# Optimization experiments

Hardware: AMD Instinct MI355X
Metric: run time of the kernel (lower is better)

The kernel has to match this reference:

```python
import jax, jax.numpy as jnp
import numpy as np

HIDDEN = 2048
NUM_HEADS = 32
NUM_KV_HEADS = 4
HEAD_DIM = 128
EPS = 1e-6
ROPE_THETA = 10000.0
Q_SIZE = NUM_HEADS * HEAD_DIM      # 4096
KV_SIZE = NUM_KV_HEADS * HEAD_DIM  # 512


def setup_inputs() -> dict:
    key = jax.random.key(0)
    k1, k2, k3, k4, k5 = jax.random.split(key, 5)
    T = 2048
    hidden_states = jax.random.normal(k1, (T, HIDDEN), dtype=jnp.float32)
    positions = jnp.arange(T, dtype=jnp.int64)
    # qkv_proj weight: [q_size + 2*kv_size, hidden] (torch Linear convention)
    w_qkv = jax.random.normal(k2, (Q_SIZE + 2 * KV_SIZE, HIDDEN), dtype=jnp.float32) * (HIDDEN ** -0.5)
    # o_proj weight: [hidden, num_heads*head_dim]
    w_o = jax.random.normal(k3, (HIDDEN, Q_SIZE), dtype=jnp.float32) * (Q_SIZE ** -0.5)
    q_norm_w = jnp.ones((HEAD_DIM,), dtype=jnp.float32) + 0.1 * jax.random.normal(k4, (HEAD_DIM,), dtype=jnp.float32)
    k_norm_w = jnp.ones((HEAD_DIM,), dtype=jnp.float32) + 0.1 * jax.random.normal(k5, (HEAD_DIM,), dtype=jnp.float32)
    return {"positions": positions, "hidden_states": hidden_states,
            "w_qkv": w_qkv, "w_o": w_o, "q_norm_w": q_norm_w, "k_norm_w": k_norm_w}


def _rms_norm(x, w):
    # x: [..., head_dim]; normalize over last dim
    var = jnp.mean(jnp.square(x), axis=-1, keepdims=True)
    return x * jax.lax.rsqrt(var + EPS) * w


def _rope(positions, x):
    # neox-style rotary over full head_dim. x: [T, H, D]
    half = HEAD_DIM // 2
    inv_freq = 1.0 / (ROPE_THETA ** (jnp.arange(0, half, dtype=jnp.float32) / half))
    freqs = positions.astype(jnp.float32)[:, None] * inv_freq[None, :]  # [T, half]
    cos = jnp.cos(freqs)[:, None, :]  # [T, 1, half]
    sin = jnp.sin(freqs)[:, None, :]
    x1, x2 = x[..., :half], x[..., half:]
    return jnp.concatenate([x1 * cos - x2 * sin, x2 * cos + x1 * sin], axis=-1)


def reference(positions, hidden_states, w_qkv, w_o, q_norm_w, k_norm_w):
    T = hidden_states.shape[0]
    qkv = hidden_states @ w_qkv.T  # [T, q_size+2*kv_size]
    q, k, v = jnp.split(qkv, [Q_SIZE, Q_SIZE + KV_SIZE], axis=-1)
    q = _rms_norm(q.reshape(T, NUM_HEADS, HEAD_DIM), q_norm_w)
    k = _rms_norm(k.reshape(T, NUM_KV_HEADS, HEAD_DIM), k_norm_w)
    v = v.reshape(T, NUM_KV_HEADS, HEAD_DIM)
    q = _rope(positions, q)
    k = _rope(positions, k)
    # GQA: expand kv heads to query heads
    rep = NUM_HEADS // NUM_KV_HEADS
    k = jnp.repeat(k, rep, axis=1)  # [T, H, D]
    v = jnp.repeat(v, rep, axis=1)
    scale = HEAD_DIM ** -0.5
    scores = jnp.einsum('qhd,khd->hqk', q, k) * scale  # [H, T, T]
    causal = jnp.tril(jnp.ones((T, T), dtype=bool))
    scores = jnp.where(causal[None, :, :], scores, jnp.float32(-1e30))
    probs = jax.nn.softmax(scores, axis=-1)
    attn = jnp.einsum('hqk,khd->qhd', probs, v).reshape(T, Q_SIZE)
    return attn @ w_o.T  # [T, hidden]
```

## Files before the change

### kernel.cpp

```cpp
#include <hip/hip_runtime.h>

#define T_TOK   2048
#define HID     2048
#define NHEADS  32
#define NKV     4
#define HD      128
#define QSZ     4096
#define KVSZ    512
#define QKVW    5120

typedef unsigned short u16;
typedef __bf16 bf16x8 __attribute__((ext_vector_type(8)));
typedef float  f32x4  __attribute__((ext_vector_type(4)));

__device__ __forceinline__ u16 f2bf(float f) {
  unsigned int u = __float_as_uint(f);
  u += 0x7fffu + ((u >> 16) & 1u);
  return (u16)(u >> 16);
}

__device__ __forceinline__ u16 f2bf_n(float f) {
  __bf16 h = (__bf16)f;
  return __builtin_bit_cast(u16, h);
}

__device__ __forceinline__ float bf2f(u16 u) {
  return __uint_as_float((unsigned int)u << 16);
}

__device__ __forceinline__ void gl2lds16(const void* g, void* l) {
  __builtin_amdgcn_global_load_lds(
      (const __attribute__((address_space(1))) unsigned int*)g,
      (__attribute__((address_space(3))) unsigned int*)l, 16, 0, 0);
}

template<int N>
__device__ __forceinline__ float rotmax(float x) {
  int t = __builtin_amdgcn_mov_dpp(__float_as_int(x), 0x120 | N, 0xf, 0xf, true);
  return fmaxf(x, __int_as_float(t));
}
template<int N>
__device__ __forceinline__ float rotadd(float x) {
  int t = __builtin_amdgcn_mov_dpp(__float_as_int(x), 0x120 | N, 0xf, 0xf, true);
  return x + __int_as_float(t);
}

__global__ void cvt3_f32_bf16(const float* __restrict__ in0, u16* __restrict__ o0, int n0,
                              const float* __restrict__ in1, u16* __restrict__ o1, int n1,
                              const float* __restrict__ in2, u16* __restrict__ o2, int n2) {
  int i = blockIdx.x * blockDim.x + threadIdx.x;
  const float* in; u16* out;
  if (i < n0)            { in = in0; out = o0; }
  else if (i < n0 + n1)  { in = in1; out = o1; i -= n0; }
  else if (i < n0+n1+n2) { in = in2; out = o2; i -= n0 + n1; }
  else return;
  float4 v = ((const float4*)in)[i];
  ushort4 o;
  o.x = f2bf(v.x); o.y = f2bf(v.y); o.z = f2bf(v.z); o.w = f2bf(v.w);
  ((ushort4*)out)[i] = o;
}

template<int BM, bool OUT16>
__launch_bounds__(256, 4)
__global__ void gemm_nt(const u16* __restrict__ A, const u16* __restrict__ B,
                        void* __restrict__ Cv, int M, int N, int K) {
  constexpr int MI = BM / 32;
  __shared__ __align__(16) u16 As[2][BM * 32];
  __shared__ __align__(16) u16 Bs[2][128 * 32];
  const int tid  = threadIdx.x;
  const int wave = tid >> 6, lane = tid & 63;
  const int l15  = lane & 15, quad = lane >> 4;
  const int wr   = wave >> 1, wc = wave & 1;

  const int nwg = gridDim.x * gridDim.y;
  int lid = blockIdx.y * gridDim.x + blockIdx.x;
  lid = (lid & 7) * (nwg >> 3) + (lid >> 3);
  const int bx = lid % gridDim.x;
  const int by = lid / gridDim.x;

  const u16* Ab = A + (size_t)by * BM * K;
  const u16* Bb = B + (size_t)bx * 128 * K;

  f32x4 acc[MI][4];
#pragma unroll
  for (int i = 0; i < MI; i++)
#pragma unroll
    for (int j = 0; j < 4; j++) acc[i][j] = (f32x4){0.f, 0.f, 0.f, 0.f};

  constexpr int ACH = BM * 32 / 8;
  auto stage = [&](int t, int buf) {
    const int k0 = t * 32;
#pragma unroll
    for (int s = 0; s < (ACH + 512) / 256; s++) {
      int c = tid + s * 256;
      if (c < ACH) {
        int row = c >> 2, co = (c & 3) * 8;
        gl2lds16(Ab + (size_t)row * K + k0 + co, &As[buf][c * 8]);
      } else {
        int c2 = c - ACH;
        int row = c2 >> 2, co = (c2 & 3) * 8;
        gl2lds16(Bb + (size_t)row * K + k0 + co, &Bs[buf][c2 * 8]);
      }
    }
  };

  const int nst = K / 32;
  stage(0, 0);

  for (int t = 0; t < nst; t++) {
    const int cur = t & 1;
    __syncthreads();
    if (t + 1 < nst) stage(t + 1, cur ^ 1);

    bf16x8 af[MI], bf[4];
#pragma unroll
    for (int i = 0; i < MI; i++) af[i] = *(const bf16x8*)&As[cur][(wr * (BM / 2) + i * 16 + l15) * 32 + quad * 8];
#pragma unroll
    for (int j = 0; j < 4; j++) bf[j] = *(const bf16x8*)&Bs[cur][(wc * 64 + j * 16 + l15) * 32 + quad * 8];
#pragma unroll
    for (int i = 0; i < MI; i++)
#pragma unroll
      for (int j = 0; j < 4; j++)
        acc[i][j] = __builtin_amdgcn_mfma_f32_16x16x32_bf16(af[i], bf[j], acc[i][j], 0, 0, 0);
  }

#pragma unroll
  for (int i = 0; i < MI; i++) {
    int rbase = wr * (BM / 2) + i * 16 + quad * 4;
#pragma unroll
    for (int j = 0; j < 4; j++) {
      int col = wc * 64 + j * 16 + l15;
#pragma unroll
      for (int r = 0; r < 4; r++) {
        size_t idx = (size_t)(by * BM + rbase + r) * N + bx * 128 + col;
        if constexpr (OUT16) ((u16*)Cv)[idx] = f2bf_n(acc[i][j][r]);
        else                 ((float*)Cv)[idx] = acc[i][j][r];
      }
    }
  }
}

__global__ void norm_rope(const u16* __restrict__ qkv, const int* __restrict__ pos,
                          const float* __restrict__ qw, const float* __restrict__ kw,
                          u16* __restrict__ qB, u16* __restrict__ kB, u16* __restrict__ vB) {
  const int t = blockIdx.x;
  const int wave = threadIdx.x >> 6, l = threadIdx.x & 63;
  const u16* row = qkv + (size_t)t * QKVW;

  constexpr float QSC = 0.08838834764831845f * 1.4426950408889634f;

  const float p = (float)pos[t];
  const float fr = p * exp2f(-(float)l * 0.20762050593046014f);
  float sn, cs;
  sincosf(fr, &sn, &cs);

  for (int slot = wave; slot < 40; slot += 4) {
    if (slot < 36) {
      const int   base = (slot < 32) ? slot * 128 : 4096 + (slot - 32) * 128;
      const float* w   = (slot < 32) ? qw : kw;
      float x1 = bf2f(row[base + l]), x2 = bf2f(row[base + 64 + l]);
      float ss = x1 * x1 + x2 * x2;
      ss = rotadd<1>(ss); ss = rotadd<2>(ss); ss = rotadd<4>(ss); ss = rotadd<8>(ss);
      ss += __shfl_xor(ss, 16);
      ss += __shfl_xor(ss, 32);
      float rs = rsqrtf(ss * (1.f / 128.f) + 1e-6f);
      float n1 = x1 * rs * w[l], n2 = x2 * rs * w[64 + l];
      float o1 = n1 * cs - n2 * sn;
      float o2 = n2 * cs + n1 * sn;
      if (slot < 32) {
        o1 *= QSC;
        o2 *= QSC;
        qB[(size_t)t * QSZ + slot * 128 + l]      = f2bf(o1);
        qB[(size_t)t * QSZ + slot * 128 + 64 + l] = f2bf(o2);
      } else {
        kB[(size_t)t * KVSZ + (slot - 32) * 128 + l]      = f2bf(o1);
        kB[(size_t)t * KVSZ + (slot - 32) * 128 + 64 + l] = f2bf(o2);
      }
    } else {
      int vh = slot - 36;
      vB[(size_t)t * KVSZ + vh * 128 + l]      = row[4608 + vh * 128 + l];
      vB[(size_t)t * KVSZ + vh * 128 + 64 + l] = row[4608 + vh * 128 + 64 + l];
    }
  }
}

__global__ void transpose_v(const u16* __restrict__ vB, u16* __restrict__ vT) {
  __shared__ u16 Ld[64 * 65];
  const int tb = blockIdx.x;
  const int db = blockIdx.y;
  const int tid = threadIdx.x;
  const int r  = tid >> 3;
  const int c8 = (tid & 7) * 8;
#pragma unroll
  for (int s = 0; s < 2; s++) {
    int tr = r + s * 32;
    uint4 v = *(const uint4*)&vB[(size_t)(tb * 64 + tr) * KVSZ + db * 64 + c8];
    const u16* pv = (const u16*)&v;
#pragma unroll
    for (int j = 0; j < 8; j++) Ld[tr * 65 + c8 + j] = pv[j];
  }
  __syncthreads();
#pragma unroll
  for (int s = 0; s < 2; s++) {
    int dr = r + s * 32;
    uint4 v; u16* pv = (u16*)&v;
#pragma unroll
    for (int j = 0; j < 8; j++) pv[j] = Ld[(c8 + j) * 65 + dr];
    *(uint4*)&vT[(size_t)(db * 64 + dr) * T_TOK + tb * 64 + c8] = v;
  }
}

__launch_bounds__(512, 4)
__global__ void attn_fa(const u16* __restrict__ qB, const u16* __restrict__ kB,
                        const u16* __restrict__ vT, u16* __restrict__ oB) {
  const int qb  = (blockIdx.y < 16) ? (15 - (int)blockIdx.x) : (int)blockIdx.x;
  const int h   = blockIdx.y;
  const int kvh = h >> 3;
  __shared__ __align__(16) u16 Kb[2][64 * 16 * 8];
  __shared__ __align__(16) u16 Vb[2][128 * 8 * 8];
  __shared__ __align__(16) u16 Pb[128 * 8 * 8];

  const int tid  = threadIdx.x;
  const int wave = tid >> 6, lane = tid & 63;
  const int l15  = lane & 15, quad = lane >> 4;

  auto stage = [&](int kt, int buf) {
#pragma unroll
    for (int s = 0; s < 2; s++) {
      int c = tid + s * 512;
      int r = c >> 4;
      gl2lds16(kB + (size_t)(kt * 64 + r) * KVSZ + kvh * 128 + ((c & 15) ^ (r & 15)) * 8,
               &Kb[buf][c * 8]);
    }
#pragma unroll
    for (int s = 0; s < 2; s++) {
      int c = tid + s * 512;
      int rv = c >> 3;
      gl2lds16(vT + ((size_t)kvh * 128 + rv) * T_TOK + kt * 64 + ((c & 7) ^ (rv & 7)) * 8,
               &Vb[buf][c * 8]);
    }
  };

  bf16x8 qf[4];
#pragma unroll
  for (int ds = 0; ds < 4; ds++)
    qf[ds] = *(const bf16x8*)(qB + (size_t)(qb * 128 + wave * 16 + l15) * QSZ
                                 + h * 128 + ds * 32 + quad * 8);

  f32x4 o[8];
#pragma unroll
  for (int ni = 0; ni < 8; ni++) o[ni] = (f32x4){0.f, 0.f, 0.f, 0.f};
  float mrow[4], lrow[4];
#pragma unroll
  for (int r = 0; r < 4; r++) { mrow[r] = -3.0e38f; lrow[r] = 0.f; }

  const int nt = 2 * qb + 2;

  stage(0, 0);

  for (int kt = 0; kt < nt; kt++) {
    const int cur = kt & 1;
    __syncthreads();
    if (kt + 1 < nt) stage(kt + 1, cur ^ 1);

    f32x4 sc[4];
#pragma unroll
    for (int ni = 0; ni < 4; ni++) sc[ni] = (f32x4){0.f, 0.f, 0.f, 0.f};
    __builtin_amdgcn_s_setprio(1);
#pragma unroll
    for (int ds = 0; ds < 4; ds++) {
#pragma unroll
      for (int ni = 0; ni < 4; ni++) {
        bf16x8 kf = *(const bf16x8*)&Kb[cur][((ni * 16 + l15) * 16 + ((ds * 4 + quad) ^ l15)) * 8];
        sc[ni] = __builtin_amdgcn_mfma_f32_16x16x32_bf16(qf[ds], kf, sc[ni], 0, 0, 0);
      }
    }
    __builtin_amdgcn_s_setprio(0);

    if (kt >= 2 * qb) {
#pragma unroll
      for (int ni = 0; ni < 4; ni++)
#pragma unroll
        for (int r = 0; r < 4; r++) {
          int key = kt * 64 + ni * 16 + l15;
          int rw  = qb * 128 + wave * 16 + quad * 4 + r;
          if (key > rw) sc[ni][r] = -1.0e30f;
        }
    }

#pragma unroll
    for (int r = 0; r < 4; r++) {
      float mx = fmaxf(fmaxf(sc[0][r], sc[1][r]), fmaxf(sc[2][r], sc[3][r]));
      mx = rotmax<1>(mx); mx = rotmax<2>(mx); mx = rotmax<4>(mx); mx = rotmax<8>(mx);
      if (!__all(mx <= mrow[r] + 8.f)) {
        float mn = fmaxf(mrow[r], mx);
        float al = exp2f(mrow[r] - mn);
        mrow[r]  = mn;
        lrow[r] *= al;
#pragma unroll
        for (int ni = 0; ni < 8; ni++) o[ni][r] *= al;
      }
      float rs = 0.f;
#pragma unroll
      for (int ni = 0; ni < 4; ni++) {
        float pv = exp2f(sc[ni][r] - mrow[r]);
        sc[ni][r] = pv;
        rs += pv;
      }
      lrow[r] += rs;
    }

#pragma unroll
    for (int ni = 0; ni < 4; ni++)
#pragma unroll
      for (int r = 0; r < 4; r++) {
        int row = wave * 16 + quad * 4 + r;
        Pb[(row * 8 + ((ni * 2 + (l15 >> 3)) ^ (row & 7))) * 8 + (l15 & 7)] =
            f2bf_n(sc[ni][r]);
      }

    __builtin_amdgcn_s_setprio(1);
#pragma unroll
    for (int ks = 0; ks < 2; ks++) {
      bf16x8 pf = *(const bf16x8*)&Pb[((wave * 16 + l15) * 8 + ((ks * 4 + quad) ^ (l15 & 7))) * 8];
#pragma unroll
      for (int ni = 0; ni < 8; ni++) {
        bf16x8 vf = *(const bf16x8*)&Vb[cur][((ni * 16 + l15) * 8 + ((ks * 4 + quad) ^ (l15 & 7))) * 8];
        o[ni] = __builtin_amdgcn_mfma_f32_16x16x32_bf16(pf, vf, o[ni], 0, 0, 0);
      }
    }
    __builtin_amdgcn_s_setprio(0);
  }

#pragma unroll
  for (int r = 0; r < 4; r++) {
    float s = lrow[r];
    s = rotadd<1>(s); s = rotadd<2>(s); s = rotadd<4>(s); s = rotadd<8>(s);
    float rinv = 1.0f / s;
    int t = qb * 128 + wave * 16 + quad * 4 + r;
#pragma unroll
    for (int ni = 0; ni < 8; ni++)
      oB[(size_t)t * QSZ + h * 128 + ni * 16 + l15] = f2bf_n(o[ni][r] * rinv);
  }
}

extern "C" void kernel_launch(void* const* d_in, const int* in_sizes, int n_in,
                              void* d_out, int out_size, void* d_ws, size_t ws_size,
                              hipStream_t stream) {
  const int*   positions = (const int*)d_in[0];
  const float* hidden    = (const float*)d_in[1];
  const float* w_qkv     = (const float*)d_in[2];
  const float* w_o       = (const float*)d_in[3];
  const float* qw        = (const float*)d_in[4];
  const float* kw        = (const float*)d_in[5];
  float* out = (float*)d_out;
  char*  ws  = (char*)d_ws;

  u16* hiddenB = (u16*)ws;
  u16* wqkvB   = hiddenB + (size_t)HID * HID;
  u16* woB     = wqkvB + (size_t)QKVW * HID;
  size_t off1  = ((size_t)HID * HID + (size_t)QKVW * HID + (size_t)HID * QSZ) * 2;
  u16* qkvB    = (u16*)(ws + off1);
  u16* attnB   = (u16*)(ws + off1);
  size_t off2  = off1 + (size_t)T_TOK * QKVW * 4;
  u16* qBuf = (u16*)(ws + off2);
  size_t off3  = off2 + (size_t)T_TOK * QSZ * 2;
  u16* kBuf = (u16*)(ws + off3);
  size_t off4  = off3 + (size_t)T_TOK * KVSZ * 2;
  u16* vTb  = (u16*)(ws + off4);
  size_t off5  = off4 + (size_t)T_TOK * KVSZ * 2;
  u16* vBuf = (u16*)(ws + off5);

  const int n0 = HID * HID / 4, n1 = QKVW * HID / 4, n2 = HID * QSZ / 4;
  cvt3_f32_bf16<<<(n0 + n1 + n2 + 255) / 256, 256, 0, stream>>>(
      hidden, hiddenB, n0, w_qkv, wqkvB, n1, w_o, woB, n2);

  gemm_nt<128, true><<<dim3(QKVW / 128, T_TOK / 128), 256, 0, stream>>>(
      hiddenB, wqkvB, qkvB, T_TOK, QKVW, HID);

  norm_rope<<<T_TOK, 256, 0, stream>>>(qkvB, positions, qw, kw, qBuf, kBuf, vBuf);

  transpose_v<<<dim3(T_TOK / 64, KVSZ / 64), 256, 0, stream>>>(vBuf, vTb);

  attn_fa<<<dim3(T_TOK / 128, NHEADS), 512, 0, stream>>>(qBuf, kBuf, vTb, attnB);

  gemm_nt<64, false><<<dim3(HID / 128, T_TOK / 64), 256, 0, stream>>>(
      attnB, woB, out, T_TOK, HID, QSZ);
}
```

Before: 344.2 us.

## Shrink attention blocks to 64 queries, balance causal work, prefetch KV through registers

The attention kernel now uses 256-thread blocks covering 64 query rows, launched as a flat 1024-block grid. Query tiles are assigned in a mirrored order so that long and short causal tiles are interleaved across slots to balance load. K/V staging changes from asynchronous global-to-LDS double buffering to register prefetch into a single LDS buffer, with an extra barrier per iteration. Separately, the V copy in norm_rope is removed and transpose_v reads V straight from the qkv buffer, which drops one intermediate write and read. The trade-off is more blocks and more re-reading of K/V, plus lost async-copy overlap, in exchange for finer-grained scheduling.

```diff
diff --git a/kernel.cpp b/kernel.cpp
--- a/kernel.cpp
+++ b/kernel.cpp
@@ -142,7 +142,7 @@
 
 __global__ void norm_rope(const u16* __restrict__ qkv, const int* __restrict__ pos,
                           const float* __restrict__ qw, const float* __restrict__ kw,
-                          u16* __restrict__ qB, u16* __restrict__ kB, u16* __restrict__ vB) {
+                          u16* __restrict__ qB, u16* __restrict__ kB) {
   const int t = blockIdx.x;
   const int wave = threadIdx.x >> 6, l = threadIdx.x & 63;
   const u16* row = qkv + (size_t)t * QKVW;
@@ -154,37 +154,31 @@
   float sn, cs;
   sincosf(fr, &sn, &cs);
 
-  for (int slot = wave; slot < 40; slot += 4) {
-    if (slot < 36) {
-      const int   base = (slot < 32) ? slot * 128 : 4096 + (slot - 32) * 128;
-      const float* w   = (slot < 32) ? qw : kw;
-      float x1 = bf2f(row[base + l]), x2 = bf2f(row[base + 64 + l]);
-      float ss = x1 * x1 + x2 * x2;
-      ss = rotadd<1>(ss); ss = rotadd<2>(ss); ss = rotadd<4>(ss); ss = rotadd<8>(ss);
-      ss += __shfl_xor(ss, 16);
-      ss += __shfl_xor(ss, 32);
-      float rs = rsqrtf(ss * (1.f / 128.f) + 1e-6f);
-      float n1 = x1 * rs * w[l], n2 = x2 * rs * w[64 + l];
-      float o1 = n1 * cs - n2 * sn;
-      float o2 = n2 * cs + n1 * sn;
-      if (slot < 32) {
-        o1 *= QSC;
-        o2 *= QSC;
-        qB[(size_t)t * QSZ + slot * 128 + l]      = f2bf(o1);
-        qB[(size_t)t * QSZ + slot * 128 + 64 + l] = f2bf(o2);
-      } else {
-        kB[(size_t)t * KVSZ + (slot - 32) * 128 + l]      = f2bf(o1);
-        kB[(size_t)t * KVSZ + (slot - 32) * 128 + 64 + l] = f2bf(o2);
-      }
+  for (int slot = wave; slot < 36; slot += 4) {
+    const int   base = (slot < 32) ? slot * 128 : 4096 + (slot - 32) * 128;
+    const float* w   = (slot < 32) ? qw : kw;
+    float x1 = bf2f(row[base + l]), x2 = bf2f(row[base + 64 + l]);
+    float ss = x1 * x1 + x2 * x2;
+    ss = rotadd<1>(ss); ss = rotadd<2>(ss); ss = rotadd<4>(ss); ss = rotadd<8>(ss);
+    ss += __shfl_xor(ss, 16);
+    ss += __shfl_xor(ss, 32);
+    float rs = rsqrtf(ss * (1.f / 128.f) + 1e-6f);
+    float n1 = x1 * rs * w[l], n2 = x2 * rs * w[64 + l];
+    float o1 = n1 * cs - n2 * sn;
+    float o2 = n2 * cs + n1 * sn;
+    if (slot < 32) {
+      o1 *= QSC;
+      o2 *= QSC;
+      qB[(size_t)t * QSZ + slot * 128 + l]      = f2bf(o1);
+      qB[(size_t)t * QSZ + slot * 128 + 64 + l] = f2bf(o2);
     } else {
-      int vh = slot - 36;
-      vB[(size_t)t * KVSZ + vh * 128 + l]      = row[4608 + vh * 128 + l];
-      vB[(size_t)t * KVSZ + vh * 128 + 64 + l] = row[4608 + vh * 128 + 64 + l];
-    }
-  }
-}
-
-__global__ void transpose_v(const u16* __restrict__ vB, u16* __restrict__ vT) {
+      kB[(size_t)t * KVSZ + (slot - 32) * 128 + l]      = f2bf(o1);
+      kB[(size_t)t * KVSZ + (slot - 32) * 128 + 64 + l] = f2bf(o2);
+    }
+  }
+}
+
+__global__ void transpose_v(const u16* __restrict__ qkv, u16* __restrict__ vT) {
   __shared__ u16 Ld[64 * 65];
   const int tb = blockIdx.x;
   const int db = blockIdx.y;
@@ -194,7 +188,7 @@
 #pragma unroll
   for (int s = 0; s < 2; s++) {
     int tr = r + s * 32;
-    uint4 v = *(const uint4*)&vB[(size_t)(tb * 64 + tr) * KVSZ + db * 64 + c8];
+    uint4 v = *(const uint4*)&qkv[(size_t)(tb * 64 + tr) * QKVW + 4608 + db * 64 + c8];
     const u16* pv = (const u16*)&v;
 #pragma unroll
     for (int j = 0; j < 8; j++) Ld[tr * 65 + c8 + j] = pv[j];
@@ -210,41 +204,34 @@
   }
 }
 
-__launch_bounds__(512, 4)
+__launch_bounds__(256, 3)
 __global__ void attn_fa(const u16* __restrict__ qB, const u16* __restrict__ kB,
                         const u16* __restrict__ vT, u16* __restrict__ oB) {
-  const int qb  = (blockIdx.y < 16) ? (15 - (int)blockIdx.x) : (int)blockIdx.x;
-  const int h   = blockIdx.y;
+  const int b    = blockIdx.x;
+  const int slot = b >> 8, k8 = b & 255;
+  const int h    = k8 & 31, g = k8 >> 5;
+  int p;
+  if      (slot == 0) p = 31 - g;
+  else if (slot == 1) p = g;
+  else if (slot == 2) p = 23 - g;
+  else                p = 8 + g;
   const int kvh = h >> 3;
-  __shared__ __align__(16) u16 Kb[2][64 * 16 * 8];
-  __shared__ __align__(16) u16 Vb[2][128 * 8 * 8];
-  __shared__ __align__(16) u16 Pb[128 * 8 * 8];
+
+  __shared__ __align__(16) u16 Kb[64 * 16 * 8];
+  __shared__ __align__(16) u16 Vb[128 * 8 * 8];
+  __shared__ __align__(16) u16 Pb[64 * 8 * 8];
 
   const int tid  = threadIdx.x;
   const int wave = tid >> 6, lane = tid & 63;
   const int l15  = lane & 15, quad = lane >> 4;
 
-  auto stage = [&](int kt, int buf) {
-#pragma unroll
-    for (int s = 0; s < 2; s++) {
-      int c = tid + s * 512;
-      int r = c >> 4;
-      gl2lds16(kB + (size_t)(kt * 64 + r) * KVSZ + kvh * 128 + ((c & 15) ^ (r & 15)) * 8,
-               &Kb[buf][c * 8]);
-    }
-#pragma unroll
-    for (int s = 0; s < 2; s++) {
-      int c = tid + s * 512;
-      int rv = c >> 3;
-      gl2lds16(vT + ((size_t)kvh * 128 + rv) * T_TOK + kt * 64 + ((c & 7) ^ (rv & 7)) * 8,
-               &Vb[buf][c * 8]);
-    }
-  };
+  const int krow = tid >> 4, kmc = tid & 15;
+  const int vrow = tid >> 3, vmc = tid & 7;
 
   bf16x8 qf[4];
 #pragma unroll
   for (int ds = 0; ds < 4; ds++)
-    qf[ds] = *(const bf16x8*)(qB + (size_t)(qb * 128 + wave * 16 + l15) * QSZ
+    qf[ds] = *(const bf16x8*)(qB + (size_t)(p * 64 + wave * 16 + l15) * QSZ
                                  + h * 128 + ds * 32 + quad * 8);
 
   f32x4 o[8];
@@ -254,14 +241,30 @@
 #pragma unroll
   for (int r = 0; r < 4; r++) { mrow[r] = -3.0e38f; lrow[r] = 0.f; }
 
-  const int nt = 2 * qb + 2;
-
-  stage(0, 0);
+  const int nt = p + 1;
+
+  uint4 kreg[4], vreg[4];
+#pragma unroll
+  for (int s = 0; s < 4; s++) {
+    kreg[s] = *(const uint4*)(kB + (size_t)(krow + s * 16) * KVSZ + kvh * 128 + kmc * 8);
+    vreg[s] = *(const uint4*)(vT + ((size_t)kvh * 128 + vrow + s * 32) * T_TOK + vmc * 8);
+  }
 
   for (int kt = 0; kt < nt; kt++) {
-    const int cur = kt & 1;
+#pragma unroll
+    for (int s = 0; s < 4; s++) {
+      int r  = krow + s * 16;
+      *(uint4*)&Kb[(r * 16 + (kmc ^ (r & 15))) * 8] = kreg[s];
+      int rv = vrow + s * 32;
+      *(uint4*)&Vb[(rv * 8 + (vmc ^ (rv & 7))) * 8] = vreg[s];
+    }
     __syncthreads();
-    if (kt + 1 < nt) stage(kt + 1, cur ^ 1);
+    const int kn = (kt + 1 < nt) ? kt + 1 : kt;
+#pragma unroll
+    for (int s = 0; s < 4; s++) {
+      kreg[s] = *(const uint4*)(kB + (size_t)(kn * 64 + krow + s * 16) * KVSZ + kvh * 128 + kmc * 8);
+      vreg[s] = *(const uint4*)(vT + ((size_t)kvh * 128 + vrow + s * 32) * T_TOK + kn * 64 + vmc * 8);
+    }
 
     f32x4 sc[4];
 #pragma unroll
@@ -271,19 +274,19 @@
     for (int ds = 0; ds < 4; ds++) {
 #pragma unroll
       for (int ni = 0; ni < 4; ni++) {
-        bf16x8 kf = *(const bf16x8*)&Kb[cur][((ni * 16 + l15) * 16 + ((ds * 4 + quad) ^ l15)) * 8];
+        bf16x8 kf = *(const bf16x8*)&Kb[((ni * 16 + l15) * 16 + ((ds * 4 + quad) ^ l15)) * 8];
         sc[ni] = __builtin_amdgcn_mfma_f32_16x16x32_bf16(qf[ds], kf, sc[ni], 0, 0, 0);
       }
     }
     __builtin_amdgcn_s_setprio(0);
 
-    if (kt >= 2 * qb) {
+    if (kt == p) {
 #pragma unroll
       for (int ni = 0; ni < 4; ni++)
 #pragma unroll
         for (int r = 0; r < 4; r++) {
           int key = kt * 64 + ni * 16 + l15;
-          int rw  = qb * 128 + wave * 16 + quad * 4 + r;
+          int rw  = p * 64 + wave * 16 + quad * 4 + r;
           if (key > rw) sc[ni][r] = -1.0e30f;
         }
     }
@@ -325,11 +328,12 @@
       bf16x8 pf = *(const bf16x8*)&Pb[((wave * 16 + l15) * 8 + ((ks * 4 + quad) ^ (l15 & 7))) * 8];
 #pragma unroll
       for (int ni = 0; ni < 8; ni++) {
-        bf16x8 vf = *(const bf16x8*)&Vb[cur][((ni * 16 + l15) * 8 + ((ks * 4 + quad) ^ (l15 & 7))) * 8];
+        bf16x8 vf = *(const bf16x8*)&Vb[((ni * 16 + l15) * 8 + ((ks * 4 + quad) ^ (l15 & 7))) * 8];
         o[ni] = __builtin_amdgcn_mfma_f32_16x16x32_bf16(pf, vf, o[ni], 0, 0, 0);
       }
     }
     __builtin_amdgcn_s_setprio(0);
+    __syncthreads();
   }
 
 #pragma unroll
@@ -337,7 +341,7 @@
     float s = lrow[r];
     s = rotadd<1>(s); s = rotadd<2>(s); s = rotadd<4>(s); s = rotadd<8>(s);
     float rinv = 1.0f / s;
-    int t = qb * 128 + wave * 16 + quad * 4 + r;
+    int t = p * 64 + wave * 16 + quad * 4 + r;
 #pragma unroll
     for (int ni = 0; ni < 8; ni++)
       oB[(size_t)t * QSZ + h * 128 + ni * 16 + l15] = f2bf_n(o[ni][r] * rinv);
@@ -368,8 +372,6 @@
   u16* kBuf = (u16*)(ws + off3);
   size_t off4  = off3 + (size_t)T_TOK * KVSZ * 2;
   u16* vTb  = (u16*)(ws + off4);
-  size_t off5  = off4 + (size_t)T_TOK * KVSZ * 2;
-  u16* vBuf = (u16*)(ws + off5);
 
   const int n0 = HID * HID / 4, n1 = QKVW * HID / 4, n2 = HID * QSZ / 4;
   cvt3_f32_bf16<<<(n0 + n1 + n2 + 255) / 256, 256, 0, stream>>>(
@@ -378,11 +380,11 @@
   gemm_nt<128, true><<<dim3(QKVW / 128, T_TOK / 128), 256, 0, stream>>>(
       hiddenB, wqkvB, qkvB, T_TOK, QKVW, HID);
 
-  norm_rope<<<T_TOK, 256, 0, stream>>>(qkvB, positions, qw, kw, qBuf, kBuf, vBuf);
-
-  transpose_v<<<dim3(T_TOK / 64, KVSZ / 64), 256, 0, stream>>>(vBuf, vTb);
-
-  attn_fa<<<dim3(T_TOK / 128, NHEADS), 512, 0, stream>>>(qBuf, kBuf, vTb, attnB);
+  norm_rope<<<T_TOK, 256, 0, stream>>>(qkvB, positions, qw, kw, qBuf, kBuf);
+
+  transpose_v<<<dim3(T_TOK / 64, KVSZ / 64), 256, 0, stream>>>(qkvB, vTb);
+
+  attn_fa<<<dim3(1024), 256, 0, stream>>>(qBuf, kBuf, vTb, attnB);
 
   gemm_nt<64, false><<<dim3(HID / 128, T_TOK / 64), 256, 0, stream>>>(
       attnB, woB, out, T_TOK, HID, QSZ);
```

Result: slower. 467.5 us (+35.8%).
